# Kernel tuning notes

Hardware: AMD Instinct MI355X
Metric: run time of the kernel (lower is better)

## Reference

```python
import jax, jax.numpy as jnp
import numpy as np

CONT_F, CATE_F = 13, 26
F = CONT_F + CATE_F            # 39 total fields
D = 40                         # orig_embedding_dim
COMB = F * (F - 1) // 2        # 741 pairs
VOCAB = 100000
B = 2048
SUB0, SUB1 = 40, 5             # subnet layer sizes
H = 100                        # hidden dims
ROWS, COLS = np.triu_indices(F, k=1)  # pair index lists (i<j)


def _ln(x, w, b, eps=1e-5):
    m = jnp.mean(x, axis=-1, keepdims=True)
    v = jnp.mean((x - m) ** 2, axis=-1, keepdims=True)
    return (x - m) * jax.lax.rsqrt(v + eps) * w + b


def setup_inputs() -> dict:
    key = jax.random.key(0)
    ks = jax.random.split(key, 12)
    s = 0.05
    first_in = COMB * SUB1 + F * D  # 3705 + 1560 = 5265
    return {
        "conts": jax.random.uniform(ks[0], (B, CONT_F), jnp.float32),
        "cates": jax.random.randint(ks[1], (B, CATE_F), 0, VOCAB),
        "combs": 0,
        "emb": jax.random.normal(ks[2], (VOCAB, D), jnp.float32) * 0.01,
        "sub_w0": jax.random.normal(ks[3], (COMB, 3 * D, SUB0), jnp.float32) * s,
        "sub_b0": jax.random.normal(ks[4], (COMB, 1, SUB0), jnp.float32) * s,
        "sln0_w": jnp.ones((SUB0,), jnp.float32),
        "sln0_b": jnp.zeros((SUB0,), jnp.float32),
        "sub_w1": jax.random.normal(ks[5], (COMB, SUB0, SUB1), jnp.float32) * s,
        "sub_b1": jax.random.normal(ks[6], (COMB, 1, SUB1), jnp.float32) * s,
        "sln1_w": jnp.ones((SUB1,), jnp.float32),
        "sln1_b": jnp.zeros((SUB1,), jnp.float32),
        "fc0_w": jax.random.normal(ks[7], (first_in, H), jnp.float32) * 0.02,
        "fc0_b": jnp.zeros((H,), jnp.float32),
        "ln0_w": jnp.ones((H,), jnp.float32),
        "ln0_b": jnp.zeros((H,), jnp.float32),
        "fc1_w": jax.random.normal(ks[8], (H, H), jnp.float32) * 0.1,
        "fc1_b": jnp.zeros((H,), jnp.float32),
        "ln1_w": jnp.ones((H,), jnp.float32),
        "ln1_b": jnp.zeros((H,), jnp.float32),
        "out_w": jax.random.normal(ks[9], (H, 1), jnp.float32) * 0.1,
        "out_b": jnp.zeros((1,), jnp.float32),
    }


def reference(conts, cates, combs, emb, sub_w0, sub_b0, sln0_w, sln0_b,
              sub_w1, sub_b1, sln1_w, sln1_b, fc0_w, fc0_b, ln0_w, ln0_b,
              fc1_w, fc1_b, ln1_w, ln1_b, out_w, out_b):
    bsz = conts.shape[0]
    # continuous fields: rows 0..CONT_F-1 of the shared embedding table scaled by value
    cont_e = emb[:CONT_F][None, :, :] * conts[:, :, None]   # [B, 13, 40]
    cate_e = emb[cates]                                      # [B, 26, 40]
    e = jnp.concatenate([cont_e, cate_e], axis=1)            # [B, 39, 40]
    # gather feature pairs
    p = e[:, ROWS]                                           # [B, 741, 40]
    q = e[:, COLS]                                           # [B, 741, 40]
    z = jnp.concatenate([p, q, p * q], axis=2)               # [B, 741, 120]
    z = jnp.transpose(z, (1, 0, 2))                          # [741, B, 120]
    # per-pair micro-MLP with shared LayerNorm params + ReLU
    z = jax.nn.relu(_ln(jnp.einsum('cbi,cio->cbo', z, sub_w0) + sub_b0, sln0_w, sln0_b))
    z = jax.nn.relu(_ln(jnp.einsum('cbi,cio->cbo', z, sub_w1) + sub_b1, sln1_w, sln1_b))
    z = jnp.transpose(z, (1, 0, 2)).reshape(bsz, -1)         # [B, 3705]
    X = jnp.concatenate([e.reshape(bsz, -1), z], axis=1)     # [B, 5265]
    X = jax.nn.relu(_ln(X @ fc0_w + fc0_b, ln0_w, ln0_b))
    X = jax.nn.relu(_ln(X @ fc1_w + fc1_b, ln1_w, ln1_b))
    return jax.nn.sigmoid(X @ out_w + out_b)                 # [B, 1]
```

## Files before the change

### kernel.cpp

```cpp
#include <hip/hip_runtime.h>

#define CONT_F 13
#define CATE_F 26
#define FF 39
#define DD 40
#define NCOMB 741
#define BB 2048
#define SUB0 40
#define SUB1 5
#define HH 100
#define K0 1560
#define KTOT 5265
#define NPART 15
#define KCH 351
#define CPX 93


__global__ __launch_bounds__(256) void build_eT_kernel(
    const float* __restrict__ conts, const int* __restrict__ cates,
    const float* __restrict__ emb, float* __restrict__ XT)
{
    const int f = blockIdx.x;
    const int b = blockIdx.y * 256 + threadIdx.x;
    float* xo = XT + (size_t)(f * DD) * BB + b;
    if (f < CONT_F) {
        const float cv = conts[b * CONT_F + f];
        const float* em = emb + f * DD;
        #pragma unroll
        for (int d = 0; d < DD; ++d)
            xo[(size_t)d * BB] = em[d] * cv;
    } else {
        const int tok = cates[b * CATE_F + (f - CONT_F)];
        const float4* er = (const float4*)(emb + (size_t)tok * DD);
        #pragma unroll
        for (int d4 = 0; d4 < DD / 4; ++d4) {
            const float4 v = er[d4];
            xo[(size_t)(d4 * 4 + 0) * BB] = v.x;
            xo[(size_t)(d4 * 4 + 1) * BB] = v.y;
            xo[(size_t)(d4 * 4 + 2) * BB] = v.z;
            xo[(size_t)(d4 * 4 + 3) * BB] = v.w;
        }
    }
}

__global__ __launch_bounds__(128) void subnetT_kernel(
    const float* __restrict__ XT, const float* __restrict__ w0,
    const float* __restrict__ b0, const float* __restrict__ sln0w,
    const float* __restrict__ sln0b, const float* __restrict__ w1,
    const float* __restrict__ b1, const float* __restrict__ sln1w,
    const float* __restrict__ sln1b, float* __restrict__ XTz)
{
    const int wgid   = blockIdx.x;
    const int xcd    = wgid & 7;
    const int within = wgid >> 3;
    const int c_loc  = within % CPX;
    const int tl     = within / CPX;
    const int c      = xcd * CPX + c_loc;
    if (c >= NCOMB) return;
    const int col = tl * 256 + threadIdx.x * 2;

    int r = 0, rem = c;
    while (rem >= FF - 1 - r) { rem -= FF - 1 - r; ++r; }
    const int s = r + 1 + rem;

    const float* Pr = XT + (size_t)(r * DD) * BB + col;
    const float* Qr = XT + (size_t)(s * DD) * BB + col;
    const float* wc = w0 + c * (3 * DD * SUB0);
    const float* bc = b0 + c * SUB0;

    float acc0[SUB0], acc1[SUB0];
    #pragma unroll
    for (int o = 0; o < SUB0; ++o) { acc0[o] = bc[o]; acc1[o] = bc[o]; }

    #pragma unroll 4
    for (int d = 0; d < DD; ++d) {
        const float2 pv = *(const float2*)(Pr + (size_t)d * BB);
        const float2 qv = *(const float2*)(Qr + (size_t)d * BB);
        const float pq0 = pv.x * qv.x, pq1 = pv.y * qv.y;
        const float* wA = wc + d * SUB0;
        #pragma unroll
        for (int o = 0; o < SUB0; ++o) {
            const float wp = wA[o], wq = wA[1600 + o], wx = wA[3200 + o];
            float a0 = acc0[o], a1 = acc1[o];
            a0 = fmaf(wp, pv.x, a0);  a1 = fmaf(wp, pv.y, a1);
            a0 = fmaf(wq, qv.x, a0);  a1 = fmaf(wq, qv.y, a1);
            a0 = fmaf(wx, pq0, a0);   a1 = fmaf(wx, pq1, a1);
            acc0[o] = a0; acc1[o] = a1;
        }
    }

    #define LN40(acc) { \
        float m = 0.f; \
        _Pragma("unroll") for (int o = 0; o < SUB0; ++o) m += acc[o]; \
        m *= (1.f / SUB0); \
        float v = 0.f; \
        _Pragma("unroll") for (int o = 0; o < SUB0; ++o) { const float dl = acc[o] - m; v += dl * dl; } \
        v *= (1.f / SUB0); \
        const float inv = rsqrtf(v + 1e-5f); \
        _Pragma("unroll") for (int o = 0; o < SUB0; ++o) { \
            const float t = (acc[o] - m) * inv * sln0w[o] + sln0b[o]; \
            acc[o] = t > 0.f ? t : 0.f; } }
    LN40(acc0)
    LN40(acc1)
    #undef LN40

    const float* w1c = w1 + c * (SUB0 * SUB1);
    float a20[SUB1], a21[SUB1];
    #pragma unroll
    for (int j = 0; j < SUB1; ++j) { a20[j] = b1[c * SUB1 + j]; a21[j] = a20[j]; }
    #pragma unroll
    for (int k = 0; k < SUB0; ++k) {
        #pragma unroll
        for (int j = 0; j < SUB1; ++j) {
            const float wv = w1c[k * SUB1 + j];
            a20[j] = fmaf(wv, acc0[k], a20[j]);
            a21[j] = fmaf(wv, acc1[k], a21[j]);
        }
    }

    #define LN5(a2) { \
        float m2 = 0.f; \
        _Pragma("unroll") for (int j = 0; j < SUB1; ++j) m2 += a2[j]; \
        m2 *= (1.f / SUB1); \
        float v2 = 0.f; \
        _Pragma("unroll") for (int j = 0; j < SUB1; ++j) { const float dl = a2[j] - m2; v2 += dl * dl; } \
        v2 *= (1.f / SUB1); \
        const float inv2 = rsqrtf(v2 + 1e-5f); \
        _Pragma("unroll") for (int j = 0; j < SUB1; ++j) \
            a2[j] = fmaxf((a2[j] - m2) * inv2 * sln1w[j] + sln1b[j], 0.f); }
    LN5(a20)
    LN5(a21)
    #undef LN5

    float* zo = XTz + (size_t)(K0 + c * SUB1) * BB + col;
    #pragma unroll
    for (int j = 0; j < SUB1; ++j) {
        float2 st; st.x = a20[j]; st.y = a21[j];
        *(float2*)(zo + (size_t)j * BB) = st;
    }
}

__global__ __launch_bounds__(256) void fc0_partialT_kernel(
    const float* __restrict__ XT, const float* __restrict__ w,
    float* __restrict__ partial)
{
    __shared__ float st[64][105];
    const int rt   = blockIdx.x;
    const int kc   = blockIdx.y;
    const int rloc = threadIdx.x & 63;
    const int ob   = __builtin_amdgcn_readfirstlane((threadIdx.x >> 6) * 25);
    const int row  = rt * 64 + rloc;

    const float* xr = XT + (size_t)(kc * KCH) * BB + row;
    const float* wr = w + (size_t)(kc * KCH) * HH + ob;

    float acc[25];
    #pragma unroll
    for (int j = 0; j < 25; ++j) acc[j] = 0.f;

    #pragma unroll 3
    for (int i = 0; i < KCH; ++i) {
        const float xv = xr[(size_t)i * BB];
        const float* wk = wr + (size_t)i * HH;
        #pragma unroll
        for (int j = 0; j < 25; ++j) acc[j] = fmaf(wk[j], xv, acc[j]);
    }
    #pragma unroll
    for (int j = 0; j < 25; ++j) st[rloc][ob + j] = acc[j];
    __syncthreads();

    float* po = partial + ((size_t)kc * BB + rt * 64) * HH;
    #pragma unroll
    for (int k = 0; k < 25; ++k) {
        const int idx = k * 256 + threadIdx.x;
        const int rr = idx / 100, hh = idx % 100;
        po[idx] = st[rr][hh];
    }
}

__global__ __launch_bounds__(256) void fc0rh_kernel(
    const float* __restrict__ partial, const float* __restrict__ fc0b,
    const float* __restrict__ ln0w, const float* __restrict__ ln0b,
    const float* __restrict__ fc1w, const float* __restrict__ fc1b,
    const float* __restrict__ ln1w, const float* __restrict__ ln1b,
    const float* __restrict__ outw, const float* __restrict__ outb,
    float* __restrict__ out)
{
    __shared__ float xs[4][104];
    const int wl   = threadIdx.x >> 6;
    const int lane = threadIdx.x & 63;
    const int row  = blockIdx.x * 4 + wl;

    float s0 = fc0b[lane];
    float s1 = (lane < 36) ? fc0b[64 + lane] : 0.f;
    #pragma unroll
    for (int p = 0; p < NPART; ++p) {
        const float* pr = partial + ((size_t)p * BB + row) * HH;
        s0 += pr[lane];
        if (lane < 36) s1 += pr[64 + lane];
    }
    float sum = s0 + ((lane < 36) ? s1 : 0.f);
    #pragma unroll
    for (int off = 32; off; off >>= 1) sum += __shfl_xor(sum, off, 64);
    float m  = sum * 0.01f;
    float d0 = s0 - m;
    float d1 = (lane < 36) ? (s1 - m) : 0.f;
    float vs = d0 * d0 + d1 * d1;
    #pragma unroll
    for (int off = 32; off; off >>= 1) vs += __shfl_xor(vs, off, 64);
    float inv = rsqrtf(vs * 0.01f + 1e-5f);
    {
        float x0 = d0 * inv * ln0w[lane] + ln0b[lane];
        xs[wl][lane] = x0 > 0.f ? x0 : 0.f;
        if (lane < 36) {
            float x1 = d1 * inv * ln0w[64 + lane] + ln0b[64 + lane];
            xs[wl][64 + lane] = x1 > 0.f ? x1 : 0.f;
        }
    }

    float a0 = fc1b[lane];
    float a1 = (lane < 36) ? fc1b[64 + lane] : 0.f;
    for (int k = 0; k < HH; ++k) {
        const float xv = xs[wl][k];
        a0 = fmaf(fc1w[k * HH + lane], xv, a0);
        if (lane < 36) a1 = fmaf(fc1w[k * HH + 64 + lane], xv, a1);
    }
    sum = a0 + ((lane < 36) ? a1 : 0.f);
    #pragma unroll
    for (int off = 32; off; off >>= 1) sum += __shfl_xor(sum, off, 64);
    m  = sum * 0.01f;
    d0 = a0 - m;
    d1 = (lane < 36) ? (a1 - m) : 0.f;
    vs = d0 * d0 + d1 * d1;
    #pragma unroll
    for (int off = 32; off; off >>= 1) vs += __shfl_xor(vs, off, 64);
    inv = rsqrtf(vs * 0.01f + 1e-5f);

    float x0 = d0 * inv * ln1w[lane] + ln1b[lane];
    x0 = x0 > 0.f ? x0 : 0.f;
    float t = x0 * outw[lane];
    if (lane < 36) {
        float x1 = d1 * inv * ln1w[64 + lane] + ln1b[64 + lane];
        x1 = x1 > 0.f ? x1 : 0.f;
        t = fmaf(x1, outw[64 + lane], t);
    }
    #pragma unroll
    for (int off = 32; off; off >>= 1) t += __shfl_xor(t, off, 64);
    if (lane == 0) {
        const float z = t + outb[0];
        out[row] = 1.f / (1.f + expf(-z));
    }
}

extern "C" void kernel_launch(void* const* d_in, const int* in_sizes, int n_in,
                              void* d_out, int out_size, void* d_ws, size_t ws_size,
                              hipStream_t stream)
{
    const float* conts = (const float*)d_in[0];
    const int*   cates = (const int*)d_in[1];
    const float* emb   = (const float*)d_in[3];
    const float* w0    = (const float*)d_in[4];
    const float* b0    = (const float*)d_in[5];
    const float* sln0w = (const float*)d_in[6];
    const float* sln0b = (const float*)d_in[7];
    const float* w1    = (const float*)d_in[8];
    const float* b1    = (const float*)d_in[9];
    const float* sln1w = (const float*)d_in[10];
    const float* sln1b = (const float*)d_in[11];
    const float* fc0w  = (const float*)d_in[12];
    const float* fc0b  = (const float*)d_in[13];
    const float* ln0w  = (const float*)d_in[14];
    const float* ln0b  = (const float*)d_in[15];
    const float* fc1w  = (const float*)d_in[16];
    const float* fc1b  = (const float*)d_in[17];
    const float* ln1w  = (const float*)d_in[18];
    const float* ln1b  = (const float*)d_in[19];
    const float* outw  = (const float*)d_in[20];
    const float* outb  = (const float*)d_in[21];
    float* out = (float*)d_out;

    float* XT      = (float*)d_ws;
    float* partial = XT + (size_t)KTOT * BB;

    build_eT_kernel<<<dim3(FF, BB / 256), 256, 0, stream>>>(conts, cates, emb, XT);
    subnetT_kernel<<<8 * CPX * 8, 128, 0, stream>>>(
        XT, w0, b0, sln0w, sln0b, w1, b1, sln1w, sln1b, XT);
    fc0_partialT_kernel<<<dim3(BB / 64, NPART), 256, 0, stream>>>(XT, fc0w, partial);
    fc0rh_kernel<<<BB / 4, 256, 0, stream>>>(
        partial, fc0b, ln0w, ln0b, fc1w, fc1b, ln1w, ln1b, outw, outb, out);
}
```

Baseline: 392.5 us.

## Stage subnet and fc0 weights in LDS with vectorized reads and retiled fc0

The subnet kernel now copies each pair's 4800-float first-layer weight block into shared memory and reads it as float4 instead of issuing scalar global loads. It also adds an occupancy hint of 3 blocks per SM and lowers the unroll factor. The fc0 partial kernel is retiled: each block covers 128 batch rows, with each thread holding 50 accumulators. Weights are staged into padded LDS in three sub-chunks of 117 rows and read as float4, replacing the old per-thread global weight loads and the LDS transpose on output. The trade-off is roughly 19KB of LDS per subnet block, more register pressure in fc0, and half as many fc0 blocks.

```diff
diff --git a/kernel.cpp b/kernel.cpp
--- a/kernel.cpp
+++ b/kernel.cpp
@@ -13,6 +13,7 @@
 #define KTOT 5265
 #define NPART 15
 #define KCH 351
+#define KSUB 117
 #define CPX 93
 
 
@@ -43,13 +44,14 @@
     }
 }
 
-__global__ __launch_bounds__(128) void subnetT_kernel(
+__global__ __launch_bounds__(128, 3) void subnetT_kernel(
     const float* __restrict__ XT, const float* __restrict__ w0,
     const float* __restrict__ b0, const float* __restrict__ sln0w,
     const float* __restrict__ sln0b, const float* __restrict__ w1,
     const float* __restrict__ b1, const float* __restrict__ sln1w,
     const float* __restrict__ sln1b, float* __restrict__ XTz)
 {
+    __shared__ float lw[3 * DD * SUB0];
     const int wgid   = blockIdx.x;
     const int xcd    = wgid & 7;
     const int within = wgid >> 3;
@@ -59,33 +61,47 @@
     if (c >= NCOMB) return;
     const int col = tl * 256 + threadIdx.x * 2;
 
+    {
+        const float* wsrc = w0 + c * (3 * DD * SUB0);
+        for (int i = threadIdx.x; i < 3 * DD * SUB0; i += 128)
+            lw[i] = wsrc[i];
+    }
+    __syncthreads();
+
     int r = 0, rem = c;
     while (rem >= FF - 1 - r) { rem -= FF - 1 - r; ++r; }
     const int s = r + 1 + rem;
 
     const float* Pr = XT + (size_t)(r * DD) * BB + col;
     const float* Qr = XT + (size_t)(s * DD) * BB + col;
-    const float* wc = w0 + c * (3 * DD * SUB0);
     const float* bc = b0 + c * SUB0;
 
     float acc0[SUB0], acc1[SUB0];
     #pragma unroll
     for (int o = 0; o < SUB0; ++o) { acc0[o] = bc[o]; acc1[o] = bc[o]; }
 
-    #pragma unroll 4
+    #pragma unroll 2
     for (int d = 0; d < DD; ++d) {
         const float2 pv = *(const float2*)(Pr + (size_t)d * BB);
         const float2 qv = *(const float2*)(Qr + (size_t)d * BB);
         const float pq0 = pv.x * qv.x, pq1 = pv.y * qv.y;
-        const float* wA = wc + d * SUB0;
+        const float4* wp4 = (const float4*)(lw + d * SUB0);
+        const float4* wq4 = (const float4*)(lw + 1600 + d * SUB0);
+        const float4* wx4 = (const float4*)(lw + 3200 + d * SUB0);
         #pragma unroll
-        for (int o = 0; o < SUB0; ++o) {
-            const float wp = wA[o], wq = wA[1600 + o], wx = wA[3200 + o];
-            float a0 = acc0[o], a1 = acc1[o];
-            a0 = fmaf(wp, pv.x, a0);  a1 = fmaf(wp, pv.y, a1);
-            a0 = fmaf(wq, qv.x, a0);  a1 = fmaf(wq, qv.y, a1);
-            a0 = fmaf(wx, pq0, a0);   a1 = fmaf(wx, pq1, a1);
-            acc0[o] = a0; acc1[o] = a1;
+        for (int o4 = 0; o4 < SUB0 / 4; ++o4) {
+            const float4 wp = wp4[o4];
+            const float4 wq = wq4[o4];
+            const float4 wx = wx4[o4];
+            #define FMA1(comp, oo) { \
+                const int o = o4 * 4 + oo; \
+                float a0 = acc0[o], a1 = acc1[o]; \
+                a0 = fmaf(wp.comp, pv.x, a0);  a1 = fmaf(wp.comp, pv.y, a1); \
+                a0 = fmaf(wq.comp, qv.x, a0);  a1 = fmaf(wq.comp, qv.y, a1); \
+                a0 = fmaf(wx.comp, pq0, a0);   a1 = fmaf(wx.comp, pq1, a1); \
+                acc0[o] = a0; acc1[o] = a1; }
+            FMA1(x, 0) FMA1(y, 1) FMA1(z, 2) FMA1(w, 3)
+            #undef FMA1
         }
     }
 
@@ -144,37 +160,50 @@
     const float* __restrict__ XT, const float* __restrict__ w,
     float* __restrict__ partial)
 {
-    __shared__ float st[64][105];
-    const int rt   = blockIdx.x;
-    const int kc   = blockIdx.y;
-    const int rloc = threadIdx.x & 63;
-    const int ob   = __builtin_amdgcn_readfirstlane((threadIdx.x >> 6) * 25);
-    const int row  = rt * 64 + rloc;
-
-    const float* xr = XT + (size_t)(kc * KCH) * BB + row;
-    const float* wr = w + (size_t)(kc * KCH) * HH + ob;
-
-    float acc[25];
-    #pragma unroll
-    for (int j = 0; j < 25; ++j) acc[j] = 0.f;
-
-    #pragma unroll 3
-    for (int i = 0; i < KCH; ++i) {
-        const float xv = xr[(size_t)i * BB];
-        const float* wk = wr + (size_t)i * HH;
-        #pragma unroll
-        for (int j = 0; j < 25; ++j) acc[j] = fmaf(wk[j], xv, acc[j]);
-    }
-    #pragma unroll
-    for (int j = 0; j < 25; ++j) st[rloc][ob + j] = acc[j];
-    __syncthreads();
-
-    float* po = partial + ((size_t)kc * BB + rt * 64) * HH;
-    #pragma unroll
-    for (int k = 0; k < 25; ++k) {
-        const int idx = k * 256 + threadIdx.x;
-        const int rr = idx / 100, hh = idx % 100;
-        po[idx] = st[rr][hh];
+    __shared__ float ws[KSUB * 104];
+    const int bt = blockIdx.x;
+    const int kc = blockIdx.y;
+    const int l  = threadIdx.x & 127;
+    const int hg = threadIdx.x >> 7;
+    const int b  = bt * 128 + l;
+
+    float acc[50];
+    #pragma unroll
+    for (int j = 0; j < 50; ++j) acc[j] = 0.f;
+
+    for (int ph = 0; ph < 3; ++ph) {
+        const int k0 = kc * KCH + ph * KSUB;
+        __syncthreads();
+        for (int i = threadIdx.x; i < KSUB * 100; i += 256) {
+            const int rr = i / 100, h = i % 100;
+            ws[rr * 104 + (h < 50 ? h : h + 2)] = w[(size_t)(k0 + rr) * HH + h];
+        }
+        __syncthreads();
+
+        const float* xp = XT + (size_t)k0 * BB + b;
+        const float* wrow = ws + hg * 52;
+        for (int rr = 0; rr < KSUB; ++rr) {
+            const float xv = xp[(size_t)rr * BB];
+            const float4* w4 = (const float4*)(wrow + rr * 104);
+            #pragma unroll
+            for (int j4 = 0; j4 < 12; ++j4) {
+                const float4 wv = w4[j4];
+                acc[j4 * 4 + 0] = fmaf(wv.x, xv, acc[j4 * 4 + 0]);
+                acc[j4 * 4 + 1] = fmaf(wv.y, xv, acc[j4 * 4 + 1]);
+                acc[j4 * 4 + 2] = fmaf(wv.z, xv, acc[j4 * 4 + 2]);
+                acc[j4 * 4 + 3] = fmaf(wv.w, xv, acc[j4 * 4 + 3]);
+            }
+            const float2 w2 = *(const float2*)(wrow + rr * 104 + 48);
+            acc[48] = fmaf(w2.x, xv, acc[48]);
+            acc[49] = fmaf(w2.y, xv, acc[49]);
+        }
+    }
+
+    float* po = partial + ((size_t)kc * BB + b) * HH + hg * 50;
+    #pragma unroll
+    for (int j2 = 0; j2 < 25; ++j2) {
+        float2 st; st.x = acc[j2 * 2]; st.y = acc[j2 * 2 + 1];
+        *(float2*)(po + j2 * 2) = st;
     }
 }
 
@@ -285,7 +314,7 @@
     build_eT_kernel<<<dim3(FF, BB / 256), 256, 0, stream>>>(conts, cates, emb, XT);
     subnetT_kernel<<<8 * CPX * 8, 128, 0, stream>>>(
         XT, w0, b0, sln0w, sln0b, w1, b1, sln1w, sln1b, XT);
-    fc0_partialT_kernel<<<dim3(BB / 64, NPART), 256, 0, stream>>>(XT, fc0w, partial);
+    fc0_partialT_kernel<<<dim3(BB / 128, NPART), 256, 0, stream>>>(XT, fc0w, partial);
     fc0rh_kernel<<<BB / 4, 256, 0, stream>>>(
         partial, fc0b, ln0w, ln0b, fc1w, fc1b, ln1w, ln1b, outw, outb, out);
 }
```

Result: slower. 528.8 us (+34.7%).

## Run per-pair subnet layer on bf16 MFMA with split-precision emulation

Applied to the files above, without the earlier changes.

Replaces the scalar-FMA per-pair micro-MLP with a matrix-core version that splits the fp32 weights and activations into bf16 hi/lo parts and issues three MFMA products per tile to approximate fp32 accuracy. LayerNorm and the 40->5 layer are done with cross-lane shuffles on the MFMA output layout. The grid changes to two blocks per pair, each covering half the batch. This targets the FMA-bound first subnet layer, at the cost of 3x MFMA work, conversion overhead, padding of 40->48 outputs and 120->128 inputs, and strided, uncoalesced gathers of activations from the transposed buffer.

```diff
diff --git a/kernel.cpp b/kernel.cpp
--- a/kernel.cpp
+++ b/kernel.cpp
@@ -13,8 +13,18 @@
 #define KTOT 5265
 #define NPART 15
 #define KCH 351
-#define CPX 93
-
+
+using short8 = __attribute__((ext_vector_type(8))) short;
+using f32x4  = __attribute__((ext_vector_type(4))) float;
+
+__device__ __forceinline__ short f2bf(float f) {
+    unsigned u = __float_as_uint(f);
+    unsigned r = (u + 0x7FFFu + ((u >> 16) & 1u)) >> 16;
+    return (short)r;
+}
+__device__ __forceinline__ float bf2f(short h) {
+    return __uint_as_float(((unsigned)(unsigned short)h) << 16);
+}
 
 __global__ __launch_bounds__(256) void build_eT_kernel(
     const float* __restrict__ conts, const int* __restrict__ cates,
@@ -43,100 +53,168 @@
     }
 }
 
-__global__ __launch_bounds__(128) void subnetT_kernel(
+__global__ __launch_bounds__(256, 2) void subnet_mfma_kernel(
     const float* __restrict__ XT, const float* __restrict__ w0,
     const float* __restrict__ b0, const float* __restrict__ sln0w,
     const float* __restrict__ sln0b, const float* __restrict__ w1,
     const float* __restrict__ b1, const float* __restrict__ sln1w,
     const float* __restrict__ sln1b, float* __restrict__ XTz)
 {
-    const int wgid   = blockIdx.x;
-    const int xcd    = wgid & 7;
-    const int within = wgid >> 3;
-    const int c_loc  = within % CPX;
-    const int tl     = within / CPX;
-    const int c      = xcd * CPX + c_loc;
-    if (c >= NCOMB) return;
-    const int col = tl * 256 + threadIdx.x * 2;
+    const int c    = blockIdx.x >> 1;
+    const int half = blockIdx.x & 1;
+    const int t    = threadIdx.x;
+    const int w    = t >> 6;
+    const int l    = t & 63;
+    const int l15  = l & 15;
+    const int grp  = l >> 4;
 
     int r = 0, rem = c;
     while (rem >= FF - 1 - r) { rem -= FF - 1 - r; ++r; }
     const int s = r + 1 + rem;
-
-    const float* Pr = XT + (size_t)(r * DD) * BB + col;
-    const float* Qr = XT + (size_t)(s * DD) * BB + col;
-    const float* wc = w0 + c * (3 * DD * SUB0);
-    const float* bc = b0 + c * SUB0;
-
-    float acc0[SUB0], acc1[SUB0];
-    #pragma unroll
-    for (int o = 0; o < SUB0; ++o) { acc0[o] = bc[o]; acc1[o] = bc[o]; }
-
-    #pragma unroll 4
-    for (int d = 0; d < DD; ++d) {
-        const float2 pv = *(const float2*)(Pr + (size_t)d * BB);
-        const float2 qv = *(const float2*)(Qr + (size_t)d * BB);
-        const float pq0 = pv.x * qv.x, pq1 = pv.y * qv.y;
-        const float* wA = wc + d * SUB0;
-        #pragma unroll
-        for (int o = 0; o < SUB0; ++o) {
-            const float wp = wA[o], wq = wA[1600 + o], wx = wA[3200 + o];
-            float a0 = acc0[o], a1 = acc1[o];
-            a0 = fmaf(wp, pv.x, a0);  a1 = fmaf(wp, pv.y, a1);
-            a0 = fmaf(wq, qv.x, a0);  a1 = fmaf(wq, qv.y, a1);
-            a0 = fmaf(wx, pq0, a0);   a1 = fmaf(wx, pq1, a1);
-            acc0[o] = a0; acc1[o] = a1;
-        }
-    }
-
-    #define LN40(acc) { \
-        float m = 0.f; \
-        _Pragma("unroll") for (int o = 0; o < SUB0; ++o) m += acc[o]; \
-        m *= (1.f / SUB0); \
-        float v = 0.f; \
-        _Pragma("unroll") for (int o = 0; o < SUB0; ++o) { const float dl = acc[o] - m; v += dl * dl; } \
-        v *= (1.f / SUB0); \
-        const float inv = rsqrtf(v + 1e-5f); \
-        _Pragma("unroll") for (int o = 0; o < SUB0; ++o) { \
-            const float t = (acc[o] - m) * inv * sln0w[o] + sln0b[o]; \
-            acc[o] = t > 0.f ? t : 0.f; } }
-    LN40(acc0)
-    LN40(acc1)
-    #undef LN40
-
-    const float* w1c = w1 + c * (SUB0 * SUB1);
-    float a20[SUB1], a21[SUB1];
-    #pragma unroll
-    for (int j = 0; j < SUB1; ++j) { a20[j] = b1[c * SUB1 + j]; a21[j] = a20[j]; }
-    #pragma unroll
-    for (int k = 0; k < SUB0; ++k) {
-        #pragma unroll
-        for (int j = 0; j < SUB1; ++j) {
-            const float wv = w1c[k * SUB1 + j];
-            a20[j] = fmaf(wv, acc0[k], a20[j]);
-            a21[j] = fmaf(wv, acc1[k], a21[j]);
-        }
-    }
-
-    #define LN5(a2) { \
-        float m2 = 0.f; \
-        _Pragma("unroll") for (int j = 0; j < SUB1; ++j) m2 += a2[j]; \
-        m2 *= (1.f / SUB1); \
-        float v2 = 0.f; \
-        _Pragma("unroll") for (int j = 0; j < SUB1; ++j) { const float dl = a2[j] - m2; v2 += dl * dl; } \
-        v2 *= (1.f / SUB1); \
-        const float inv2 = rsqrtf(v2 + 1e-5f); \
-        _Pragma("unroll") for (int j = 0; j < SUB1; ++j) \
-            a2[j] = fmaxf((a2[j] - m2) * inv2 * sln1w[j] + sln1b[j], 0.f); }
-    LN5(a20)
-    LN5(a21)
-    #undef LN5
-
-    float* zo = XTz + (size_t)(K0 + c * SUB1) * BB + col;
-    #pragma unroll
-    for (int j = 0; j < SUB1; ++j) {
-        float2 st; st.x = a20[j]; st.y = a21[j];
-        *(float2*)(zo + (size_t)j * BB) = st;
+    const float* XTr = XT + (size_t)(r * DD) * BB;
+    const float* XTs = XT + (size_t)(s * DD) * BB;
+
+    short8 Ah[3][4], Al[3][4];
+    #pragma unroll
+    for (int mt = 0; mt < 3; ++mt) {
+        const int o = mt * 16 + l15;
+        #pragma unroll
+        for (int ks = 0; ks < 4; ++ks) {
+            short8 hh, ll;
+            #pragma unroll
+            for (int j = 0; j < 8; ++j) {
+                const int k = ks * 32 + grp * 8 + j;
+                const float v = (o < SUB0 && k < 120)
+                    ? w0[(size_t)c * 4800 + k * SUB0 + o] : 0.f;
+                const short h = f2bf(v);
+                hh[j] = h;
+                ll[j] = f2bf(v - bf2f(h));
+            }
+            Ah[mt][ks] = hh;
+            Al[mt][ks] = ll;
+        }
+    }
+
+    float b0r[3][4], slwr[3][4], slbr[3][4], w1r[3][4][5];
+    #pragma unroll
+    for (int mt = 0; mt < 3; ++mt) {
+        #pragma unroll
+        for (int rg = 0; rg < 4; ++rg) {
+            const int o = mt * 16 + grp * 4 + rg;
+            const bool re = (o < SUB0);
+            b0r[mt][rg]  = re ? b0[c * SUB0 + o]   : 0.f;
+            slwr[mt][rg] = re ? sln0w[o]           : 0.f;
+            slbr[mt][rg] = re ? sln0b[o]           : 0.f;
+            #pragma unroll
+            for (int j = 0; j < 5; ++j)
+                w1r[mt][rg][j] = re ? w1[(size_t)c * 200 + o * 5 + j] : 0.f;
+        }
+    }
+    float b1r[5], s1w[5], s1b[5];
+    #pragma unroll
+    for (int j = 0; j < 5; ++j) {
+        b1r[j] = b1[c * SUB1 + j];
+        s1w[j] = sln1w[j];
+        s1b[j] = sln1b[j];
+    }
+
+    for (int it = half * 16; it < half * 16 + 16; ++it) {
+        const int bb = it * 64 + w * 16 + l15;
+
+        f32x4 acc0 = {0.f, 0.f, 0.f, 0.f};
+        f32x4 acc1 = {0.f, 0.f, 0.f, 0.f};
+        f32x4 acc2 = {0.f, 0.f, 0.f, 0.f};
+
+        #pragma unroll
+        for (int ks = 0; ks < 4; ++ks) {
+            short8 Bh, Bl;
+            #pragma unroll
+            for (int j = 0; j < 8; ++j) {
+                const int k = ks * 32 + grp * 8 + j;
+                float v;
+                if (ks == 0) {
+                    v = XTr[(size_t)k * BB + bb];
+                } else {
+                    const int kp = (k < 40) ? k : ((k >= 80) ? k - 80 : 0);
+                    const int kq = (k >= 40) ? ((k < 80) ? k - 40 : k - 80) : 0;
+                    const float vp = XTr[(size_t)kp * BB + bb];
+                    const float vq = XTs[(size_t)kq * BB + bb];
+                    v = (k < 40) ? vp : ((k < 80) ? vq : vp * vq);
+                    if (k >= 120) v = 0.f;
+                }
+                const short h = f2bf(v);
+                Bh[j] = h;
+                Bl[j] = f2bf(v - bf2f(h));
+            }
+            acc0 = __builtin_amdgcn_mfma_f32_16x16x32_bf16(Ah[0][ks], Bh, acc0, 0, 0, 0);
+            acc1 = __builtin_amdgcn_mfma_f32_16x16x32_bf16(Ah[1][ks], Bh, acc1, 0, 0, 0);
+            acc2 = __builtin_amdgcn_mfma_f32_16x16x32_bf16(Ah[2][ks], Bh, acc2, 0, 0, 0);
+            acc0 = __builtin_amdgcn_mfma_f32_16x16x32_bf16(Ah[0][ks], Bl, acc0, 0, 0, 0);
+            acc1 = __builtin_amdgcn_mfma_f32_16x16x32_bf16(Ah[1][ks], Bl, acc1, 0, 0, 0);
+            acc2 = __builtin_amdgcn_mfma_f32_16x16x32_bf16(Ah[2][ks], Bl, acc2, 0, 0, 0);
+            acc0 = __builtin_amdgcn_mfma_f32_16x16x32_bf16(Al[0][ks], Bh, acc0, 0, 0, 0);
+            acc1 = __builtin_amdgcn_mfma_f32_16x16x32_bf16(Al[1][ks], Bh, acc1, 0, 0, 0);
+            acc2 = __builtin_amdgcn_mfma_f32_16x16x32_bf16(Al[2][ks], Bh, acc2, 0, 0, 0);
+        }
+
+        float vv[3][4];
+        #pragma unroll
+        for (int rg = 0; rg < 4; ++rg) {
+            vv[0][rg] = acc0[rg] + b0r[0][rg];
+            vv[1][rg] = acc1[rg] + b0r[1][rg];
+            vv[2][rg] = acc2[rg] + b0r[2][rg];
+        }
+        float sum = 0.f, sq = 0.f;
+        #pragma unroll
+        for (int mt = 0; mt < 3; ++mt)
+            #pragma unroll
+            for (int rg = 0; rg < 4; ++rg) {
+                const float x = vv[mt][rg];
+                sum += x;
+                sq = fmaf(x, x, sq);
+            }
+        sum += __shfl_xor(sum, 16); sum += __shfl_xor(sum, 32);
+        sq  += __shfl_xor(sq, 16);  sq  += __shfl_xor(sq, 32);
+        const float mean = sum * 0.025f;
+        const float var  = sq * 0.025f - mean * mean;
+        const float inv  = rsqrtf(var + 1e-5f);
+
+        float p[5] = {0.f, 0.f, 0.f, 0.f, 0.f};
+        #pragma unroll
+        for (int mt = 0; mt < 3; ++mt)
+            #pragma unroll
+            for (int rg = 0; rg < 4; ++rg) {
+                const float hx = fmaxf(
+                    fmaf((vv[mt][rg] - mean) * inv, slwr[mt][rg], slbr[mt][rg]), 0.f);
+                #pragma unroll
+                for (int j = 0; j < 5; ++j)
+                    p[j] = fmaf(w1r[mt][rg][j], hx, p[j]);
+            }
+        #pragma unroll
+        for (int j = 0; j < 5; ++j) {
+            p[j] += __shfl_xor(p[j], 16);
+            p[j] += __shfl_xor(p[j], 32);
+        }
+        float a2[5];
+        float sum2 = 0.f, sq2 = 0.f;
+        #pragma unroll
+        for (int j = 0; j < 5; ++j) {
+            a2[j] = p[j] + b1r[j];
+            sum2 += a2[j];
+            sq2 = fmaf(a2[j], a2[j], sq2);
+        }
+        const float m2   = sum2 * 0.2f;
+        const float var2 = sq2 * 0.2f - m2 * m2;
+        const float inv2 = rsqrtf(var2 + 1e-5f);
+
+        if (grp == 0) {
+            float* zo = XTz + (size_t)(K0 + c * SUB1) * BB + bb;
+            #pragma unroll
+            for (int j = 0; j < 5; ++j) {
+                const float z = fmaf((a2[j] - m2) * inv2, s1w[j], s1b[j]);
+                zo[(size_t)j * BB] = z > 0.f ? z : 0.f;
+            }
+        }
     }
 }
 
@@ -283,7 +361,7 @@
     float* partial = XT + (size_t)KTOT * BB;
 
     build_eT_kernel<<<dim3(FF, BB / 256), 256, 0, stream>>>(conts, cates, emb, XT);
-    subnetT_kernel<<<8 * CPX * 8, 128, 0, stream>>>(
+    subnet_mfma_kernel<<<NCOMB * 2, 256, 0, stream>>>(
         XT, w0, b0, sln0w, sln0b, w1, b1, sln1w, sln1b, XT);
     fc0_partialT_kernel<<<dim3(BB / 64, NPART), 256, 0, stream>>>(XT, fc0w, partial);
     fc0rh_kernel<<<BB / 4, 256, 0, stream>>>(
```

New measurement: 758.6 us. 93.3% more time.
